# Performance work log

Measured on AMD Instinct MI355X. Metric: run time of the kernel, lower is better.

The kernel has to match this reference:

```python
import jax, jax.numpy as jnp
import numpy as np

ROPE_DIM = 64       # config.rope_dim
GN_GROUPS = 32      # config.group_norm_num
GN_CHANNELS = 2048  # config.group_norm_channels == intermediate_size
GN_EPS = 1e-5


def rope_rotate(x):
    """lucidrains rotary-embedding-torch rotate_queries_or_keys:
    interleaved-pair rotation of the first ROPE_DIM features, rest pass through."""
    T = x.shape[-2]
    inv_freq = 1.0 / (10000.0 ** (jnp.arange(0, ROPE_DIM, 2, dtype=jnp.float32) / ROPE_DIM))
    freqs = jnp.arange(T, dtype=jnp.float32)[:, None] * inv_freq[None, :]  # (T, ROPE_DIM/2)
    freqs = jnp.repeat(freqs, 2, axis=-1)                                  # (T, ROPE_DIM)
    cos, sin = jnp.cos(freqs), jnp.sin(freqs)
    xr = x[..., :ROPE_DIM]
    x1, x2 = xr[..., 0::2], xr[..., 1::2]
    rot = jnp.stack((-x2, x1), axis=-1).reshape(xr.shape)  # rotate_half, interleaved
    xr = xr * cos + rot * sin
    return jnp.concatenate([xr, x[..., ROPE_DIM:]], axis=-1)


def group_norm_rows(x2d, weight, bias):
    """torch GroupNorm on a 2D (N, C) input: normalize each group of channels per row."""
    N, Cc = x2d.shape
    xg = x2d.reshape(N, GN_GROUPS, Cc // GN_GROUPS)
    mu = xg.mean(-1, keepdims=True)
    var = xg.var(-1, keepdims=True)
    xn = ((xg - mu) * jax.lax.rsqrt(var + GN_EPS)).reshape(N, Cc)
    return xn * weight + bias


def setup_inputs() -> dict:
    key = jax.random.key(0)
    ks = jax.random.split(key, 4)
    B, T, I, C = 2, 4096, 2048, 2048
    X = jax.random.normal(ks[0], (B, T, I), dtype=jnp.float32)
    S_n = jnp.zeros((B, C), dtype=jnp.float32)
    W_Q = jax.random.normal(ks[1], (I, C), dtype=jnp.float32) / I
    hh_b = jax.random.normal(ks[2], (C,), dtype=jnp.float32) * 0.02  # nn.Linear bias of self.hh
    gn_weight = jnp.ones((C,), dtype=jnp.float32)
    gn_bias = jnp.zeros((C,), dtype=jnp.float32)
    return {"X": X, "S_n": S_n, "W_Q": W_Q, "hh_b": hh_b,
            "gn_weight": gn_weight, "gn_bias": gn_bias}


def reference(X, S_n, W_Q, hh_b, gn_weight, gn_bias):
    # forward_auto_rec with chunk_len = T (single chunk, h_t starts at zeros):
    #   Q = ReLU(rope(X @ W_Q));  H = tanh(hh(0) + Q) = tanh(Q + b_hh)
    # K, V and the decay-masked A = (H K^T * D) V are computed in the source but
    # discarded (out = H), so they are dead code (DCE'd under jit) and omitted.
    B, T, _ = X.shape
    Q = jax.nn.relu(rope_rotate(X @ W_Q))   # (B, T, C)
    H = jnp.tanh(Q + hh_b)                  # (B, T, C)
    C = H.shape[-1]
    # dropout in eval mode = identity
    out = group_norm_rows(H.reshape(-1, C), gn_weight, gn_bias).reshape(B, T, C)
    # out.transpose(-2,-1).contiguous().view(B,T,C): reshape of the transposed layout
    out = jnp.swapaxes(out, -2, -1).reshape(B, T, C)
    return out, S_n
```

## Files before the change

kernel.cpp:

```cpp
#include <hip/hip_runtime.h>

#define T_DIM 4096
#define C_DIM 2048
#define K_DIM 2048

typedef __bf16 bf16x8 __attribute__((ext_vector_type(8)));
typedef float f32x4 __attribute__((ext_vector_type(4)));

__device__ __forceinline__ unsigned short f2bf(float f) {
  union { float f; unsigned int i; } x;
  x.f = f;
  unsigned int r = x.i + 0x7fffu + ((x.i >> 16) & 1u);
  return (unsigned short)(r >> 16);
}

#define GLD16(gsrc, ldst)                                                   \
  __builtin_amdgcn_global_load_lds(                                         \
      (const __attribute__((address_space(1))) unsigned int*)(gsrc),        \
      (__attribute__((address_space(3))) unsigned int*)(ldst), 16, 0, 0)

__global__ __launch_bounds__(256) void transpose_w(const float* __restrict__ W,
                                                   unsigned short* __restrict__ Wt) {
  __shared__ float tile[64][68];
  const int c0 = blockIdx.x * 64;
  const int r0 = blockIdx.y * 64;
  const int tid = threadIdx.x;
#pragma unroll
  for (int i = 0; i < 4; ++i) {
    int s = tid + i * 256;
    int r = s >> 4, c4 = (s & 15) * 4;
    *(float4*)&tile[r][c4] = *(const float4*)&W[(size_t)(r0 + r) * C_DIM + c0 + c4];
  }
  __syncthreads();
#pragma unroll
  for (int i = 0; i < 2; ++i) {
    int s = tid + i * 256;
    int n = s >> 3, k8 = (s & 7) * 8;
    __align__(16) unsigned short tmp[8];
#pragma unroll
    for (int j = 0; j < 8; ++j) tmp[j] = f2bf(tile[k8 + j][n]);
    *(uint4*)&Wt[(size_t)(c0 + n) * K_DIM + r0 + k8] = *(uint4*)tmp;
  }
}

__global__ __launch_bounds__(256) void cvt_x(const float* __restrict__ X,
                                             unsigned short* __restrict__ Xb) {
  size_t base = (size_t)blockIdx.x * 2048 + (size_t)threadIdx.x * 8;
  float4 a = *(const float4*)&X[base];
  float4 b = *(const float4*)&X[base + 4];
  __align__(16) unsigned short t[8];
  t[0] = f2bf(a.x); t[1] = f2bf(a.y); t[2] = f2bf(a.z); t[3] = f2bf(a.w);
  t[4] = f2bf(b.x); t[5] = f2bf(b.y); t[6] = f2bf(b.z); t[7] = f2bf(b.w);
  *(uint4*)&Xb[base] = *(const uint4*)t;
}

#define FOR_MN(OP) \
  OP(0,0) OP(0,1) OP(0,2) OP(0,3) \
  OP(1,0) OP(1,1) OP(1,2) OP(1,3) \
  OP(2,0) OP(2,1) OP(2,2) OP(2,3) \
  OP(3,0) OP(3,1) OP(3,2) OP(3,3)

#define DECL_ACC(m,n) f32x4 a##m##n = {0.f, 0.f, 0.f, 0.f};

template <bool ABF16>
__global__ __launch_bounds__(256, 3) void gemm_fused(const void* __restrict__ Av,
                                                     const unsigned short* __restrict__ Wt,
                                                     const float* __restrict__ hhb,
                                                     const float* __restrict__ gnw,
                                                     const float* __restrict__ gnb,
                                                     float* __restrict__ out) {
  constexpr int SMEM_BYTES = ABF16 ? 34816 : 49152;
  __shared__ __align__(16) char smem[SMEM_BYTES];
  unsigned short* lsA = (unsigned short*)smem;
  float* lsAf = (float*)smem;
  unsigned short* lsB = (unsigned short*)(smem + (ABF16 ? 16384 : 32768));
  float(*lsO)[68] = (float(*)[68])smem;

  const int tid = threadIdx.x;
  const int wave = tid >> 6;
  const int lane = tid & 63;
  const int quad = lane >> 4;
  const int l16 = lane & 15;
  const int wm = wave >> 1, wn = wave & 1;

  const int bid = blockIdx.x;
  const int wg = (bid & 7) * 128 + (bid >> 3);
  const int m0 = (wg >> 4) * 128;
  const int n0 = (wg & 15) * 128;

  FOR_MN(DECL_ACC)

  const int srow16 = lane >> 2;
  const int scol16 = (((lane & 3) ^ (srow16 & 3)) * 8);
  const int srow32 = lane >> 3;
  const int scol32 = (((lane & 7) ^ srow32) * 4);

  const unsigned short* gA16 =
      ABF16 ? (const unsigned short*)Av + (size_t)(m0 + wave * 32 + srow16) * K_DIM + scol16
            : (const unsigned short*)0;
  const float* gA32 =
      ABF16 ? (const float*)0
            : (const float*)Av + (size_t)(m0 + wave * 32 + srow32) * K_DIM + scol32;
  const unsigned short* gB16 =
      Wt + (size_t)(n0 + wave * 32 + srow16) * K_DIM + scol16;

  const int axs = (quad ^ (l16 & 3)) * 8;
  const int abase = (wm * 64 + l16) * 32 + axs;
  const int bbase = (wn * 64 + l16) * 32 + axs;
  const int abasef = (wm * 64 + l16) * 32;
  const int u0 = ((2 * quad) ^ (l16 & 7)) * 4;
  const int u1 = ((2 * quad + 1) ^ (l16 & 7)) * 4;

  auto stage = [&](int d, int koff) {
    if constexpr (ABF16) {
      GLD16(gA16 + koff, lsA + d * 4096 + wave * 1024);
      GLD16(gA16 + koff + 16 * K_DIM, lsA + d * 4096 + wave * 1024 + 512);
    } else {
      GLD16(gA32 + koff, lsAf + d * 4096 + wave * 1024);
      GLD16(gA32 + koff + 8 * K_DIM, lsAf + d * 4096 + wave * 1024 + 256);
      GLD16(gA32 + koff + 16 * K_DIM, lsAf + d * 4096 + wave * 1024 + 512);
      GLD16(gA32 + koff + 24 * K_DIM, lsAf + d * 4096 + wave * 1024 + 768);
    }
    GLD16(gB16 + koff, lsB + d * 4096 + wave * 1024);
    GLD16(gB16 + koff + 16 * K_DIM, lsB + d * 4096 + wave * 1024 + 512);
  };

  constexpr int NT = K_DIM / 32;

  stage(0, 0);
  for (int t = 0; t < NT; ++t) {
    const int cur = t & 1;
    if (t + 1 < NT) {
      stage(cur ^ 1, (t + 1) * 32);
      if constexpr (ABF16)
        asm volatile("s_waitcnt vmcnt(4)" ::: "memory");
      else
        asm volatile("s_waitcnt vmcnt(6)" ::: "memory");
    } else {
      asm volatile("s_waitcnt vmcnt(0)" ::: "memory");
    }
    __builtin_amdgcn_s_barrier();
    asm volatile("" ::: "memory");

    const unsigned short* pa = lsA + cur * 4096;
    const float* paf = lsAf + cur * 4096;
    const unsigned short* pb = lsB + cur * 4096;

#define LOAD_AF(m)                                                        \
    bf16x8 af##m;                                                         \
    if constexpr (ABF16) {                                                \
      af##m = *(const bf16x8*)(const void*)(pa + abase + m * 512);        \
    } else {                                                              \
      const float* ap_ = paf + abasef + m * 512;                          \
      f32x4 a0_ = *(const f32x4*)(ap_ + u0);                              \
      f32x4 a1_ = *(const f32x4*)(ap_ + u1);                              \
      af##m[0] = (__bf16)a0_[0]; af##m[1] = (__bf16)a0_[1];               \
      af##m[2] = (__bf16)a0_[2]; af##m[3] = (__bf16)a0_[3];               \
      af##m[4] = (__bf16)a1_[0]; af##m[5] = (__bf16)a1_[1];               \
      af##m[6] = (__bf16)a1_[2]; af##m[7] = (__bf16)a1_[3];               \
    }
#define LOAD_BF(n)                                                        \
    bf16x8 bfr##n = *(const bf16x8*)(const void*)(pb + bbase + n * 512);

    LOAD_AF(0) LOAD_AF(1) LOAD_AF(2) LOAD_AF(3)
    LOAD_BF(0) LOAD_BF(1) LOAD_BF(2) LOAD_BF(3)

#define MFMA_OP(m,n) \
    a##m##n = __builtin_amdgcn_mfma_f32_16x16x32_bf16(af##m, bfr##n, a##m##n, 0, 0, 0);
    FOR_MN(MFMA_OP)
#undef LOAD_AF
#undef LOAD_BF

    asm volatile("s_waitcnt lgkmcnt(0)" ::: "memory");
    __builtin_amdgcn_sched_barrier(0);
    __builtin_amdgcn_s_barrier();
    asm volatile("" ::: "memory");
  }

  const int c_base = n0 + wn * 64;
  const int t_base = (m0 & (T_DIM - 1)) + wm * 64;

#define LOADC(n)                                  \
  const int c##n = c_base + n * 16 + l16;         \
  const float hb##n = hhb[c##n];                  \
  const float gw##n = gnw[c##n];                  \
  const float gb##n = gnb[c##n];
  LOADC(0) LOADC(1) LOADC(2) LOADC(3)

  if (c_base == 0) {
#define ROPE_E(n,m,r)                                                   \
    { float v_ = a##m##n[r];                                            \
      float p_ = __shfl_xor(v_, 1, 64);                                 \
      int t_ = t_base + m * 16 + quad * 4 + r;                          \
      float ang_ = (float)t_ * fr_;                                     \
      float s_ = sinf(ang_);                                            \
      float co_ = cosf(ang_);                                           \
      a##m##n[r] = v_ * co_ + sg_ * p_ * s_; }
#define ROPE_M(n,m) ROPE_E(n,m,0) ROPE_E(n,m,1) ROPE_E(n,m,2) ROPE_E(n,m,3)
#define ROPE_N(n)                                                       \
    { int cc_ = n * 16 + l16;                                           \
      int ii_ = cc_ >> 1;                                               \
      float fr_ = expf(-(float)ii_ * 0.28782313662425572f);             \
      float sg_ = (cc_ & 1) ? 1.f : -1.f;                               \
      ROPE_M(n,0) ROPE_M(n,1) ROPE_M(n,2) ROPE_M(n,3) }
    ROPE_N(0) ROPE_N(1) ROPE_N(2) ROPE_N(3)
  }

#define GN_ROW(m,r)                                                     \
  { float h0_ = tanhf(fmaxf(a##m##0[r], 0.f) + hb0);                    \
    float h1_ = tanhf(fmaxf(a##m##1[r], 0.f) + hb1);                    \
    float h2_ = tanhf(fmaxf(a##m##2[r], 0.f) + hb2);                    \
    float h3_ = tanhf(fmaxf(a##m##3[r], 0.f) + hb3);                    \
    float s1_ = h0_ + h1_ + h2_ + h3_;                                  \
    float s2_ = h0_ * h0_ + h1_ * h1_ + h2_ * h2_ + h3_ * h3_;          \
    s1_ += __shfl_xor(s1_, 1, 64);  s2_ += __shfl_xor(s2_, 1, 64);      \
    s1_ += __shfl_xor(s1_, 2, 64);  s2_ += __shfl_xor(s2_, 2, 64);      \
    s1_ += __shfl_xor(s1_, 4, 64);  s2_ += __shfl_xor(s2_, 4, 64);      \
    s1_ += __shfl_xor(s1_, 8, 64);  s2_ += __shfl_xor(s2_, 8, 64);      \
    float mu_ = s1_ * 0.015625f;                                        \
    float var_ = s2_ * 0.015625f - mu_ * mu_;                           \
    float rs_ = rsqrtf(var_ + 1e-5f);                                   \
    a##m##0[r] = (h0_ - mu_) * rs_ * gw0 + gb0;                         \
    a##m##1[r] = (h1_ - mu_) * rs_ * gw1 + gb1;                         \
    a##m##2[r] = (h2_ - mu_) * rs_ * gw2 + gb2;                         \
    a##m##3[r] = (h3_ - mu_) * rs_ * gw3 + gb3; }
#define GN_M(m) GN_ROW(m,0) GN_ROW(m,1) GN_ROW(m,2) GN_ROW(m,3)
  GN_M(0) GN_M(1) GN_M(2) GN_M(3)

  const int bb = m0 >> 12;
  const int t0 = m0 & (T_DIM - 1);
#define ST_MN(m,n)                                                      \
  lsO[wn * 64 + n * 16 + l16][m * 16 + quad * 4 + 0] = a##m##n[0];      \
  lsO[wn * 64 + n * 16 + l16][m * 16 + quad * 4 + 1] = a##m##n[1];      \
  lsO[wn * 64 + n * 16 + l16][m * 16 + quad * 4 + 2] = a##m##n[2];      \
  lsO[wn * 64 + n * 16 + l16][m * 16 + quad * 4 + 3] = a##m##n[3];
#pragma unroll
  for (int h = 0; h < 2; ++h) {
    if (wm == h) {
      FOR_MN(ST_MN)
    }
    __syncthreads();
#pragma unroll
    for (int i = 0; i < 8; ++i) {
      int s = tid + i * 256;
      int cl = s >> 4;
      int t4 = (s & 15) * 4;
      float4 v = *(const float4*)&lsO[cl][t4];
      *(float4*)&out[(size_t)bb * C_DIM * T_DIM + (size_t)(n0 + cl) * T_DIM + t0 + h * 64 + t4] = v;
    }
    __syncthreads();
  }
}

__global__ __launch_bounds__(256) void copy_sn(const float* __restrict__ src,
                                               float* __restrict__ dst) {
  int i = blockIdx.x * 256 + threadIdx.x;
  dst[i] = src[i];
}

extern "C" void kernel_launch(void* const* d_in, const int* in_sizes, int n_in,
                              void* d_out, int out_size, void* d_ws, size_t ws_size,
                              hipStream_t stream) {
  const float* X = (const float*)d_in[0];
  const float* Sn = (const float*)d_in[1];
  const float* W = (const float*)d_in[2];
  const float* hhb = (const float*)d_in[3];
  const float* gnw = (const float*)d_in[4];
  const float* gnb = (const float*)d_in[5];
  float* out = (float*)d_out;

  unsigned short* Wt = (unsigned short*)d_ws;
  const size_t wt_bytes = (size_t)C_DIM * K_DIM * 2;
  const size_t xb_bytes = (size_t)2 * T_DIM * K_DIM * 2;

  transpose_w<<<dim3(32, 32), dim3(256), 0, stream>>>(W, Wt);

  if (ws_size >= wt_bytes + xb_bytes) {
    unsigned short* Xb = Wt + (size_t)C_DIM * K_DIM;
    cvt_x<<<dim3(8192), dim3(256), 0, stream>>>(X, Xb);
    gemm_fused<true><<<dim3(1024), dim3(256), 0, stream>>>(Xb, Wt, hhb, gnw, gnb, out);
  } else {
    gemm_fused<false><<<dim3(1024), dim3(256), 0, stream>>>(X, Wt, hhb, gnw, gnb, out);
  }

  copy_sn<<<dim3(16), dim3(256), 0, stream>>>(Sn, out + (size_t)16777216);
}
```

Measured before the change: 342.6 us.

## Double K-tile depth to 64 in bf16 GEMM path with wider LDS swizzle

For the bf16-A path, each pipeline stage now loads a 64-deep K slice (128x64 tiles of A and B) instead of 32, halving the number of loop iterations and barriers. The LDS layout changes to 64-element rows with an 8-way XOR swizzle, and two MFMA sub-steps run per stage. LDS use grows to 64 KB, so the occupancy hint drops from 3 to 2 blocks per CU, trading latency hiding for fewer synchronizations. The fp32-A path is kept unchanged in its own branch.

```diff
diff --git a/kernel.cpp b/kernel.cpp
--- a/kernel.cpp
+++ b/kernel.cpp
@@ -63,17 +63,17 @@
 #define DECL_ACC(m,n) f32x4 a##m##n = {0.f, 0.f, 0.f, 0.f};
 
 template <bool ABF16>
-__global__ __launch_bounds__(256, 3) void gemm_fused(const void* __restrict__ Av,
+__global__ __launch_bounds__(256, 2) void gemm_fused(const void* __restrict__ Av,
                                                      const unsigned short* __restrict__ Wt,
                                                      const float* __restrict__ hhb,
                                                      const float* __restrict__ gnw,
                                                      const float* __restrict__ gnb,
                                                      float* __restrict__ out) {
-  constexpr int SMEM_BYTES = ABF16 ? 34816 : 49152;
+  constexpr int SMEM_BYTES = ABF16 ? 65536 : 49152;
   __shared__ __align__(16) char smem[SMEM_BYTES];
   unsigned short* lsA = (unsigned short*)smem;
   float* lsAf = (float*)smem;
-  unsigned short* lsB = (unsigned short*)(smem + (ABF16 ? 16384 : 32768));
+  unsigned short* lsB = (unsigned short*)(smem + 32768);
   float(*lsO)[68] = (float(*)[68])smem;
 
   const int tid = threadIdx.x;
@@ -90,91 +90,130 @@
 
   FOR_MN(DECL_ACC)
 
-  const int srow16 = lane >> 2;
-  const int scol16 = (((lane & 3) ^ (srow16 & 3)) * 8);
-  const int srow32 = lane >> 3;
-  const int scol32 = (((lane & 7) ^ srow32) * 4);
-
-  const unsigned short* gA16 =
-      ABF16 ? (const unsigned short*)Av + (size_t)(m0 + wave * 32 + srow16) * K_DIM + scol16
-            : (const unsigned short*)0;
-  const float* gA32 =
-      ABF16 ? (const float*)0
-            : (const float*)Av + (size_t)(m0 + wave * 32 + srow32) * K_DIM + scol32;
-  const unsigned short* gB16 =
-      Wt + (size_t)(n0 + wave * 32 + srow16) * K_DIM + scol16;
-
-  const int axs = (quad ^ (l16 & 3)) * 8;
-  const int abase = (wm * 64 + l16) * 32 + axs;
-  const int bbase = (wn * 64 + l16) * 32 + axs;
-  const int abasef = (wm * 64 + l16) * 32;
-  const int u0 = ((2 * quad) ^ (l16 & 7)) * 4;
-  const int u1 = ((2 * quad + 1) ^ (l16 & 7)) * 4;
-
-  auto stage = [&](int d, int koff) {
-    if constexpr (ABF16) {
-      GLD16(gA16 + koff, lsA + d * 4096 + wave * 1024);
-      GLD16(gA16 + koff + 16 * K_DIM, lsA + d * 4096 + wave * 1024 + 512);
-    } else {
+  if constexpr (ABF16) {
+    const int srow = lane >> 3;
+    const int scol = ((lane & 7) ^ (srow & 7)) * 8;
+    const unsigned short* gA =
+        (const unsigned short*)Av + (size_t)(m0 + wave * 32 + srow) * K_DIM + scol;
+    const unsigned short* gB =
+        Wt + (size_t)(n0 + wave * 32 + srow) * K_DIM + scol;
+
+    const int xs0 = (quad * 8) ^ ((l16 & 7) << 3);
+    const int xs1 = (32 + quad * 8) ^ ((l16 & 7) << 3);
+    const int abase = (wm * 64 + l16) * 64;
+    const int bbase = (wn * 64 + l16) * 64;
+
+    auto stage = [&](int d, int koff) {
+#pragma unroll
+      for (int r = 0; r < 4; ++r)
+        GLD16(gA + (size_t)(r * 8) * K_DIM + koff, lsA + d * 8192 + wave * 2048 + r * 512);
+#pragma unroll
+      for (int r = 0; r < 4; ++r)
+        GLD16(gB + (size_t)(r * 8) * K_DIM + koff, lsB + d * 8192 + wave * 2048 + r * 512);
+    };
+
+    constexpr int NT = K_DIM / 64;
+    stage(0, 0);
+    for (int t = 0; t < NT; ++t) {
+      const int cur = t & 1;
+      if (t + 1 < NT) {
+        stage(cur ^ 1, (t + 1) * 64);
+        asm volatile("s_waitcnt vmcnt(8)" ::: "memory");
+      } else {
+        asm volatile("s_waitcnt vmcnt(0)" ::: "memory");
+      }
+      __builtin_amdgcn_s_barrier();
+      asm volatile("" ::: "memory");
+
+      const unsigned short* pa = lsA + cur * 8192;
+      const unsigned short* pb = lsB + cur * 8192;
+
+#define LOAD_AF16(m, XS) bf16x8 af##m = *(const bf16x8*)(const void*)(pa + abase + m * 1024 + XS);
+#define LOAD_BF16(n, XS) bf16x8 bfr##n = *(const bf16x8*)(const void*)(pb + bbase + n * 1024 + XS);
+#define MFMA_OP(m,n) \
+      a##m##n = __builtin_amdgcn_mfma_f32_16x16x32_bf16(af##m, bfr##n, a##m##n, 0, 0, 0);
+      {
+        LOAD_AF16(0, xs0) LOAD_AF16(1, xs0) LOAD_AF16(2, xs0) LOAD_AF16(3, xs0)
+        LOAD_BF16(0, xs0) LOAD_BF16(1, xs0) LOAD_BF16(2, xs0) LOAD_BF16(3, xs0)
+        FOR_MN(MFMA_OP)
+      }
+      {
+        LOAD_AF16(0, xs1) LOAD_AF16(1, xs1) LOAD_AF16(2, xs1) LOAD_AF16(3, xs1)
+        LOAD_BF16(0, xs1) LOAD_BF16(1, xs1) LOAD_BF16(2, xs1) LOAD_BF16(3, xs1)
+        FOR_MN(MFMA_OP)
+      }
+#undef LOAD_AF16
+#undef LOAD_BF16
+
+      asm volatile("s_waitcnt lgkmcnt(0)" ::: "memory");
+      __builtin_amdgcn_sched_barrier(0);
+      __builtin_amdgcn_s_barrier();
+      asm volatile("" ::: "memory");
+    }
+  } else {
+    const int srow32 = lane >> 3;
+    const int scol32 = (((lane & 7) ^ srow32) * 4);
+    const int srow16 = lane >> 2;
+    const int scol16 = (((lane & 3) ^ (srow16 & 3)) * 8);
+    const float* gA32 =
+        (const float*)Av + (size_t)(m0 + wave * 32 + srow32) * K_DIM + scol32;
+    const unsigned short* gB16 =
+        Wt + (size_t)(n0 + wave * 32 + srow16) * K_DIM + scol16;
+
+    const int axs = (quad ^ (l16 & 3)) * 8;
+    const int bbase = (wn * 64 + l16) * 32 + axs;
+    const int abasef = (wm * 64 + l16) * 32;
+    const int u0 = ((2 * quad) ^ (l16 & 7)) * 4;
+    const int u1 = ((2 * quad + 1) ^ (l16 & 7)) * 4;
+
+    auto stage = [&](int d, int koff) {
       GLD16(gA32 + koff, lsAf + d * 4096 + wave * 1024);
       GLD16(gA32 + koff + 8 * K_DIM, lsAf + d * 4096 + wave * 1024 + 256);
       GLD16(gA32 + koff + 16 * K_DIM, lsAf + d * 4096 + wave * 1024 + 512);
       GLD16(gA32 + koff + 24 * K_DIM, lsAf + d * 4096 + wave * 1024 + 768);
+      GLD16(gB16 + koff, lsB + d * 4096 + wave * 1024);
+      GLD16(gB16 + koff + 16 * K_DIM, lsB + d * 4096 + wave * 1024 + 512);
+    };
+
+    constexpr int NT = K_DIM / 32;
+    stage(0, 0);
+    for (int t = 0; t < NT; ++t) {
+      const int cur = t & 1;
+      if (t + 1 < NT) {
+        stage(cur ^ 1, (t + 1) * 32);
+        asm volatile("s_waitcnt vmcnt(6)" ::: "memory");
+      } else {
+        asm volatile("s_waitcnt vmcnt(0)" ::: "memory");
+      }
+      __builtin_amdgcn_s_barrier();
+      asm volatile("" ::: "memory");
+
+      const float* paf = lsAf + cur * 4096;
+      const unsigned short* pb = lsB + cur * 4096;
+
+#define LOAD_AF32(m)                                                      \
+      bf16x8 af##m;                                                       \
+      { const float* ap_ = paf + abasef + m * 512;                        \
+        f32x4 a0_ = *(const f32x4*)(ap_ + u0);                            \
+        f32x4 a1_ = *(const f32x4*)(ap_ + u1);                            \
+        af##m[0] = (__bf16)a0_[0]; af##m[1] = (__bf16)a0_[1];             \
+        af##m[2] = (__bf16)a0_[2]; af##m[3] = (__bf16)a0_[3];             \
+        af##m[4] = (__bf16)a1_[0]; af##m[5] = (__bf16)a1_[1];             \
+        af##m[6] = (__bf16)a1_[2]; af##m[7] = (__bf16)a1_[3]; }
+#define LOAD_BF32(n)                                                      \
+      bf16x8 bfr##n = *(const bf16x8*)(const void*)(pb + bbase + n * 512);
+
+      LOAD_AF32(0) LOAD_AF32(1) LOAD_AF32(2) LOAD_AF32(3)
+      LOAD_BF32(0) LOAD_BF32(1) LOAD_BF32(2) LOAD_BF32(3)
+      FOR_MN(MFMA_OP)
+#undef LOAD_AF32
+#undef LOAD_BF32
+
+      asm volatile("s_waitcnt lgkmcnt(0)" ::: "memory");
+      __builtin_amdgcn_sched_barrier(0);
+      __builtin_amdgcn_s_barrier();
+      asm volatile("" ::: "memory");
     }
-    GLD16(gB16 + koff, lsB + d * 4096 + wave * 1024);
-    GLD16(gB16 + koff + 16 * K_DIM, lsB + d * 4096 + wave * 1024 + 512);
-  };
-
-  constexpr int NT = K_DIM / 32;
-
-  stage(0, 0);
-  for (int t = 0; t < NT; ++t) {
-    const int cur = t & 1;
-    if (t + 1 < NT) {
-      stage(cur ^ 1, (t + 1) * 32);
-      if constexpr (ABF16)
-        asm volatile("s_waitcnt vmcnt(4)" ::: "memory");
-      else
-        asm volatile("s_waitcnt vmcnt(6)" ::: "memory");
-    } else {
-      asm volatile("s_waitcnt vmcnt(0)" ::: "memory");
-    }
-    __builtin_amdgcn_s_barrier();
-    asm volatile("" ::: "memory");
-
-    const unsigned short* pa = lsA + cur * 4096;
-    const float* paf = lsAf + cur * 4096;
-    const unsigned short* pb = lsB + cur * 4096;
-
-#define LOAD_AF(m)                                                        \
-    bf16x8 af##m;                                                         \
-    if constexpr (ABF16) {                                                \
-      af##m = *(const bf16x8*)(const void*)(pa + abase + m * 512);        \
-    } else {                                                              \
-      const float* ap_ = paf + abasef + m * 512;                          \
-      f32x4 a0_ = *(const f32x4*)(ap_ + u0);                              \
-      f32x4 a1_ = *(const f32x4*)(ap_ + u1);                              \
-      af##m[0] = (__bf16)a0_[0]; af##m[1] = (__bf16)a0_[1];               \
-      af##m[2] = (__bf16)a0_[2]; af##m[3] = (__bf16)a0_[3];               \
-      af##m[4] = (__bf16)a1_[0]; af##m[5] = (__bf16)a1_[1];               \
-      af##m[6] = (__bf16)a1_[2]; af##m[7] = (__bf16)a1_[3];               \
-    }
-#define LOAD_BF(n)                                                        \
-    bf16x8 bfr##n = *(const bf16x8*)(const void*)(pb + bbase + n * 512);
-
-    LOAD_AF(0) LOAD_AF(1) LOAD_AF(2) LOAD_AF(3)
-    LOAD_BF(0) LOAD_BF(1) LOAD_BF(2) LOAD_BF(3)
-
-#define MFMA_OP(m,n) \
-    a##m##n = __builtin_amdgcn_mfma_f32_16x16x32_bf16(af##m, bfr##n, a##m##n, 0, 0, 0);
-    FOR_MN(MFMA_OP)
-#undef LOAD_AF
-#undef LOAD_BF
-
-    asm volatile("s_waitcnt lgkmcnt(0)" ::: "memory");
-    __builtin_amdgcn_sched_barrier(0);
-    __builtin_amdgcn_s_barrier();
-    asm volatile("" ::: "memory");
   }
 
   const int c_base = n0 + wn * 64;
```

New measurement: 295.6 us. 1.16x faster.
